# Kernel tuning notes

Measured on AMD Instinct MI355X. Metric: run time of the kernel, lower is better.

The kernel has to match this reference:

```python
import jax, jax.numpy as jnp
import numpy as np

NEG_INF = -10000.0  # module uses inf = 10000.0, not true infinity
B, S, N_TAGS, N_LABELS, N_PATTERNS = 256, 1024, 64, 32, 4


def setup_inputs() -> dict:
    key = jax.random.key(0)
    ks = jax.random.split(key, 8)
    label_emissions = jax.random.normal(ks[0], (B, S, N_LABELS), jnp.float32)
    pattern_emissions = jax.random.normal(ks[1], (B, S, N_PATTERNS), jnp.float32)
    y = jax.random.randint(ks[2], (B, S), 0, N_TAGS)
    label_transitions = 0.1 * jax.random.normal(ks[3], (N_LABELS, N_LABELS), jnp.float32)
    tag2label = jax.random.randint(ks[4], (N_TAGS,), 0, N_LABELS)
    tag_patterns = jax.random.bernoulli(ks[5], 0.25, (N_TAGS, N_PATTERNS)).astype(jnp.float32)
    allowed = jax.random.bernoulli(ks[6], 0.5, (N_TAGS, N_TAGS))
    transition_constraints = jnp.where(allowed, 0.0, NEG_INF).astype(jnp.float32)
    start_mask = jax.random.bernoulli(ks[7], 0.3, (N_TAGS,))
    start_mask = start_mask.at[0].set(True)  # ensure at least one start tag
    return dict(label_emissions=label_emissions,
                pattern_emissions=pattern_emissions,
                y=y,
                label_transitions=label_transitions,
                tag2label=tag2label,
                tag_patterns=tag_patterns,
                transition_constraints=transition_constraints,
                start_mask=start_mask)


def _log_p(label_emissions, pattern_emissions, label_transitions,
           tag_patterns, transition_constraints, y, tag2label, start_mask):
    # per-tag potentials x: [B, S, T]
    x = label_emissions[:, :, tag2label] + pattern_emissions @ tag_patterns.T
    # _transitions(): label_transitions.view(-1)[indices] + constraints == outer gather
    transitions = label_transitions[tag2label[:, None], tag2label[None, :]] + transition_constraints  # [T, T]

    # ----- _logZ (forward algorithm, enforce_boundaries=True) -----
    init = jnp.where(start_mask[None, :], x[:, 0, :], NEG_INF)  # [B, T]

    def step(logits, xi):
        # logmmexp(logits, transitions) + xi
        new = jax.nn.logsumexp(logits[:, :, None] + transitions[None, :, :], axis=1) + xi
        return new, None

    xs = jnp.moveaxis(x[:, 1:, :], 1, 0)  # [S-1, B, T]
    final, _ = jax.lax.scan(step, init, xs)
    logZ = jax.nn.logsumexp(final, axis=1)  # [B]

    # ----- _score -----
    emission = jnp.take_along_axis(x, y[:, :, None], axis=2)[:, :, 0].sum(axis=1)  # [B]
    trans = transitions[y[:, :-1], y[:, 1:]].sum(axis=1)  # [B]
    return emission + trans - logZ


def reference(label_emissions, pattern_emissions, y, label_transitions,
              tag2label, tag_patterns, transition_constraints, start_mask):
    return _log_p(label_emissions, pattern_emissions, label_transitions,
                  tag_patterns, transition_constraints, y, tag2label, start_mask)
```

## Files before the change

### kernel.cpp

```cpp
#include <hip/hip_runtime.h>

#define LOG2E 1.4426950408889634f
#define LN2   0.6931471805599453f
#define PSC   8.0f

typedef __attribute__((ext_vector_type(8))) short bf16x8;
typedef __attribute__((ext_vector_type(4))) float f32x4;
typedef __attribute__((ext_vector_type(4))) unsigned u32x4;

__device__ __forceinline__ unsigned pk_bf16(float lo, float hi){
  unsigned r;
  asm("v_cvt_pk_bf16_f32 %0, %1, %2" : "=v"(r) : "v"(lo), "v"(hi));
  return r;
}

__device__ __forceinline__ float wave_sum64(float v){
#define DADD(ctrl) { int _t = __builtin_amdgcn_update_dpp(0, __float_as_int(v), ctrl, 0xF, 0xF, false); \
                     v = v + __int_as_float(_t); }
  DADD(0x111) DADD(0x112) DADD(0x114) DADD(0x118) DADD(0x142) DADD(0x143)
#undef DADD
  return __int_as_float(__builtin_amdgcn_readlane(__float_as_int(v), 63));
}
__device__ __forceinline__ float wave_max64(float v){
#define DMAX(ctrl) { int _t = __builtin_amdgcn_update_dpp(__float_as_int(v), __float_as_int(v), ctrl, 0xF, 0xF, false); \
                     v = fmaxf(v, __int_as_float(_t)); }
  DMAX(0x111) DMAX(0x112) DMAX(0x114) DMAX(0x118) DMAX(0x142) DMAX(0x143)
#undef DMAX
  return __int_as_float(__builtin_amdgcn_readlane(__float_as_int(v), 63));
}
__device__ __forceinline__ f32x4 vmax4(f32x4 a, f32x4 b){
  f32x4 r; r.x=fmaxf(a.x,b.x); r.y=fmaxf(a.y,b.y); r.z=fmaxf(a.z,b.z); r.w=fmaxf(a.w,b.w); return r;
}

__global__ void __launch_bounds__(512, 1)
patcrf_fwd(const float* __restrict__ le, const float* __restrict__ pe,
           const int* __restrict__ y, const float* __restrict__ lt,
           const int* __restrict__ t2l, const float* __restrict__ tp,
           const float* __restrict__ tc, const unsigned int* __restrict__ smask,
           float* __restrict__ out)
{
  const int b = blockIdx.x;
  const int tid = threadIdx.x;
  const int wv = tid >> 6;
  const int lane = tid & 63;
  const int bb = lane & 15, jj = lane >> 4;

  __shared__ __align__(16) char smem[69632];
  float* E_lds     = (float*)smem;
  float* trans_lds = (float*)(smem + 32768);
  int*   y_lds     = (int*)(smem + 49152);
  float* P_lds     = (float*)smem;
  __shared__ __align__(16) float tp_lds[256];
  __shared__ __align__(16) float pf[64];
  __shared__ int   t2l_lds[64];
  __shared__ float scpart[8];
  __shared__ float L2arr[4];

  if (tid < 64){
    t2l_lds[tid] = t2l[tid];
    *(f32x4*)(tp_lds + tid*4) = *(const f32x4*)(tp + tid*4);
  }
  const int* yb = y + b*1024;
  y_lds[tid] = yb[tid];
  y_lds[tid+512] = yb[tid+512];
  __syncthreads();
  #pragma unroll
  for (int k=0;k<8;k++){
    int idx = k*512 + tid;
    trans_lds[idx] = lt[t2l_lds[idx>>6]*32 + t2l_lds[idx&63]] + tc[idx];
  }
  __syncthreads();

  const float* leb = le + (size_t)b*1024*32;
  const float* peb = pe + (size_t)b*1024*4;

  {
    int s0 = tid*2;
    int y0 = y_lds[s0], y1 = y_lds[s0+1];
    f32x4 pA = *(const f32x4*)(peb + (size_t)s0*4);
    f32x4 pB = *(const f32x4*)(peb + (size_t)(s0+1)*4);
    f32x4 tA = *(const f32x4*)(tp_lds + y0*4);
    f32x4 tB = *(const f32x4*)(tp_lds + y1*4);
    float s = leb[(size_t)s0*32 + t2l_lds[y0]]
            + pA.x*tA.x + pA.y*tA.y + pA.z*tA.z + pA.w*tA.w
            + leb[(size_t)(s0+1)*32 + t2l_lds[y1]]
            + pB.x*tB.x + pB.y*tB.y + pB.z*tB.z + pB.w*tB.w;
    s += trans_lds[y0*64 + y1];
    if (s0+2 < 1024) s += trans_lds[y1*64 + y_lds[s0+2]];
    float sw = wave_sum64(s);
    if (lane==0) scpart[wv] = sw;
  }

  if (wv < 4){
    const int c = wv;
    u32x4 Af[4][2];
    #pragma unroll
    for (int m=0;m<4;m++){
      #pragma unroll
      for (int h=0;h<2;h++){
        unsigned uu[4];
        #pragma unroll
        for (int q=0;q<4;q++){
          int c0 = 2*q, c1 = 2*q+1;
          int sg0 = 32*h + ((c0>>2)<<4) + 4*jj + (c0&3);
          int sg1 = 32*h + ((c1>>2)<<4) + 4*jj + (c1&3);
          float w0 = __builtin_amdgcn_exp2f(trans_lds[sg0*64 + 16*m + bb]*LOG2E);
          float w1 = __builtin_amdgcn_exp2f(trans_lds[sg1*64 + 16*m + bb]*LOG2E);
          uu[q] = pk_bf16(w0, w1);
        }
        Af[m][h] = (u32x4){uu[0],uu[1],uu[2],uu[3]};
      }
    }
    f32x4 acc[4][4];
    #pragma unroll
    for (int m=0;m<4;m++){
      #pragma unroll
      for (int n=0;n<4;n++){
        f32x4 z;
        z.x = (m==n && bb==4*jj+0) ? 1.f : 0.f;
        z.y = (m==n && bb==4*jj+1) ? 1.f : 0.f;
        z.z = (m==n && bb==4*jj+2) ? 1.f : 0.f;
        z.w = (m==n && bb==4*jj+3) ? 1.f : 0.f;
        acc[m][n] = z;
      }
    }
    float L2c = 0.f;
    const f32x4 zf = {0.f,0.f,0.f,0.f};

    __syncthreads();

    for (int ep=0; ep<16; ++ep){
      const float* Eb = E_lds + (c*2 + (ep&1))*1024;
      #pragma unroll 2
      for (int s=0;s<16;s++){
        if (c==0 && ep==0 && s==0) continue;
        f32x4 ev[4];
        #pragma unroll
        for (int m=0;m<4;m++) ev[m] = *(const f32x4*)(Eb + s*64 + 16*m + 4*jj);
        u32x4 Bf[2][4];
        #pragma unroll
        for (int n=0;n<4;n++){
          #pragma unroll
          for (int h=0;h<2;h++){
            Bf[h][n] = (u32x4){
              pk_bf16(acc[2*h][n].x,   acc[2*h][n].y),
              pk_bf16(acc[2*h][n].z,   acc[2*h][n].w),
              pk_bf16(acc[2*h+1][n].x, acc[2*h+1][n].y),
              pk_bf16(acc[2*h+1][n].z, acc[2*h+1][n].w) };
          }
        }
        #pragma unroll
        for (int m=0;m<4;m++){
          #pragma unroll
          for (int n=0;n<4;n++){
            f32x4 d = __builtin_amdgcn_mfma_f32_16x16x32_bf16(
                        __builtin_bit_cast(bf16x8, Af[m][0]),
                        __builtin_bit_cast(bf16x8, Bf[0][n]), zf, 0,0,0);
            d = __builtin_amdgcn_mfma_f32_16x16x32_bf16(
                        __builtin_bit_cast(bf16x8, Af[m][1]),
                        __builtin_bit_cast(bf16x8, Bf[1][n]), d, 0,0,0);
            acc[m][n] = d * ev[m];
          }
        }
      }
      f32x4 m4 = acc[0][0];
      #pragma unroll
      for (int m=0;m<4;m++){
        #pragma unroll
        for (int n=0;n<4;n++) m4 = vmax4(m4, acc[m][n]);
      }
      float mx = fmaxf(fmaxf(m4.x,m4.y), fmaxf(m4.z,m4.w));
      mx = wave_max64(mx);
      if (mx > 0.f){
        int Ex = (int)(__float_as_uint(mx)>>23) - 127;
        if (Ex != 0){
          float scl = __uint_as_float((unsigned)(127 - Ex) << 23);
          #pragma unroll
          for (int m=0;m<4;m++){
            #pragma unroll
            for (int n=0;n<4;n++) acc[m][n] = acc[m][n]*scl;
          }
          L2c += (float)Ex;
        }
      }
      __syncthreads();
    }

    float* Pc = P_lds + c*4352;
    #pragma unroll
    for (int m=0;m<4;m++){
      #pragma unroll
      for (int n=0;n<4;n++){
        Pc[(16*m+4*jj+0)*68 + 16*n + bb] = acc[m][n].x;
        Pc[(16*m+4*jj+1)*68 + 16*n + bb] = acc[m][n].y;
        Pc[(16*m+4*jj+2)*68 + 16*n + bb] = acc[m][n].z;
        Pc[(16*m+4*jj+3)*68 + 16*n + bb] = acc[m][n].w;
      }
    }
    if (lane==0) L2arr[c] = L2c;

  } else {
    const int c = wv - 4;
    const int myl = t2l_lds[lane];
    const f32x4 myt = *(const f32x4*)(tp_lds + lane*4);
    float leA[16]; f32x4 peA[16];
    #pragma unroll
    for (int s=0;s<16;s++){
      int t = 256*c + s;
      leA[s] = leb[(size_t)t*32 + myl];
      peA[s] = *(const f32x4*)(peb + (size_t)t*4);
    }
    #pragma unroll
    for (int s=0;s<16;s++){
      float x2 = (leA[s] + peA[s].x*myt.x + peA[s].y*myt.y
                         + peA[s].z*myt.z + peA[s].w*myt.w)*LOG2E - PSC;
      E_lds[(c*2+0)*1024 + s*64 + lane] = __builtin_amdgcn_exp2f(x2);
    }
    #pragma unroll
    for (int s=0;s<16;s++){
      int t = 256*c + 16 + s;
      leA[s] = leb[(size_t)t*32 + myl];
      peA[s] = *(const f32x4*)(peb + (size_t)t*4);
    }
    __syncthreads();

    for (int ep=0; ep<16; ++ep){
      if (ep < 15){
        float* Eh = E_lds + (c*2 + ((ep+1)&1))*1024;
        #pragma unroll
        for (int s=0;s<16;s++){
          float x2 = (leA[s] + peA[s].x*myt.x + peA[s].y*myt.y
                             + peA[s].z*myt.z + peA[s].w*myt.w)*LOG2E - PSC;
          Eh[s*64 + lane] = __builtin_amdgcn_exp2f(x2);
        }
        if (ep < 14){
          #pragma unroll
          for (int s=0;s<16;s++){
            int t = 256*c + 16*(ep+2) + s;
            leA[s] = leb[(size_t)t*32 + myl];
            peA[s] = *(const f32x4*)(peb + (size_t)t*4);
          }
        }
      }
      __syncthreads();
    }
  }
  __syncthreads();

  if (wv == 0){
    bool all01 = true, allf = true;
    #pragma unroll
    for (int k=0;k<16;k++){
      unsigned v = smask[k];
      all01 = all01 && (v <= 1u);
      allf  = allf  && (v == 0u || v == 0x3F800000u);
    }
    int startv;
    if (all01)      startv = ((const int*)smask)[lane];
    else if (allf)  startv = (((const unsigned*)smask)[lane] != 0u) ? 1 : 0;
    else            startv = ((const unsigned char*)smask)[lane];

    const int myl0 = t2l_lds[lane];
    const f32x4 myt0 = *(const f32x4*)(tp_lds + lane*4);
    f32x4 pe0 = *(const f32x4*)peb;
    float x0 = leb[myl0] + pe0.x*myt0.x + pe0.y*myt0.y + pe0.z*myt0.z + pe0.w*myt0.w;
    float v = startv ? __builtin_amdgcn_exp2f(x0*LOG2E - PSC) : 0.f;
    float L2p = 0.f;

    #pragma unroll 1
    for (int cc=0; cc<4; ++cc){
      pf[lane] = v;
      __builtin_amdgcn_wave_barrier();
      asm volatile("" ::: "memory");
      const float* Pr = P_lds + cc*4352 + lane*68;
      float q = 0.f;
      #pragma unroll
      for (int k=0;k<16;k++){
        f32x4 vv = *(const f32x4*)(pf + 4*k);
        f32x4 pp = *(const f32x4*)(Pr + 4*k);
        q = fmaf(vv.x, pp.x, q); q = fmaf(vv.y, pp.y, q);
        q = fmaf(vv.z, pp.z, q); q = fmaf(vv.w, pp.w, q);
      }
      __builtin_amdgcn_wave_barrier();
      asm volatile("" ::: "memory");
      float S = wave_sum64(q);
      L2p += __builtin_amdgcn_logf(S);
      v = q * __builtin_amdgcn_rcpf(S);
    }
    if (lane == 0){
      float sct = (scpart[0]+scpart[1])+(scpart[2]+scpart[3])
                + (scpart[4]+scpart[5])+(scpart[6]+scpart[7]);
      float l2t = (L2arr[0]+L2arr[1])+(L2arr[2]+L2arr[3]);
      float logZ = LN2 * (l2t + L2p + PSC*1024.0f);
      out[b] = sct - logZ;
    }
  }
}

extern "C" void kernel_launch(void* const* d_in, const int* in_sizes, int n_in,
                              void* d_out, int out_size, void* d_ws, size_t ws_size,
                              hipStream_t stream)
{
  patcrf_fwd<<<256, 512, 0, stream>>>(
    (const float*)d_in[0],
    (const float*)d_in[1],
    (const int*)d_in[2],
    (const float*)d_in[3],
    (const int*)d_in[4],
    (const float*)d_in[5],
    (const float*)d_in[6],
    (const unsigned int*)d_in[7],
    (float*)d_out);
}
```

Baseline: 119.9 us.

## Split each MFMA wave's chunk into two interleaved independent matrix-product chains

Each of the four MFMA waves now carries two independent 64x64 transition-product accumulators covering two 128-step sub-chunks, interleaving their MFMA chains so one chain's dependent work can hide the other's latency. The producer waves compute emissions for both sub-chunks per epoch, and the epoch count halves. The final partial products are stored to LDS as bf16 so eight matrices fit, and the combine wave now walks eight chunks. This raises register pressure, and the bf16 storage of products adds rounding error.

```diff
diff --git a/kernel.cpp b/kernel.cpp
--- a/kernel.cpp
+++ b/kernel.cpp
@@ -12,6 +12,10 @@
   unsigned r;
   asm("v_cvt_pk_bf16_f32 %0, %1, %2" : "=v"(r) : "v"(lo), "v"(hi));
   return r;
+}
+__device__ __forceinline__ unsigned short bf16_rne(float x){
+  unsigned u = __float_as_uint(x);
+  return (unsigned short)((u + 0x7FFFu + ((u>>16)&1u)) >> 16);
 }
 
 __device__ __forceinline__ float wave_sum64(float v){
@@ -45,16 +49,16 @@
   const int lane = tid & 63;
   const int bb = lane & 15, jj = lane >> 4;
 
-  __shared__ __align__(16) char smem[69632];
-  float* E_lds     = (float*)smem;
-  float* trans_lds = (float*)(smem + 32768);
-  int*   y_lds     = (int*)(smem + 49152);
-  float* P_lds     = (float*)smem;
+  __shared__ __align__(16) char smem[86016];
+  float* trans_lds = (float*)smem;
+  int*   y_lds     = (int*)(smem + 16384);
+  float* E_lds     = (float*)(smem + 20480);
+  unsigned short* P_lds = (unsigned short*)smem;
   __shared__ __align__(16) float tp_lds[256];
   __shared__ __align__(16) float pf[64];
   __shared__ int   t2l_lds[64];
   __shared__ float scpart[8];
-  __shared__ float L2arr[4];
+  __shared__ float L2arr[8];
 
   if (tid < 64){
     t2l_lds[tid] = t2l[tid];
@@ -73,6 +77,8 @@
 
   const float* leb = le + (size_t)b*1024*32;
   const float* peb = pe + (size_t)b*1024*4;
+  const int   myl  = t2l_lds[lane];
+  const f32x4 mytp = *(const f32x4*)(tp_lds + lane*4);
 
   {
     int s0 = tid*2;
@@ -91,6 +97,60 @@
     if (lane==0) scpart[wv] = sw;
   }
 
+#define CSTEP(ACC, EPTR) do { \
+    f32x4 ev[4]; \
+    _Pragma("unroll") \
+    for (int m_=0;m_<4;m_++) ev[m_] = *(const f32x4*)((EPTR) + 16*m_ + 4*jj); \
+    u32x4 Bf[2][4]; \
+    _Pragma("unroll") \
+    for (int n_=0;n_<4;n_++){ \
+      _Pragma("unroll") \
+      for (int h_=0;h_<2;h_++){ \
+        Bf[h_][n_] = (u32x4){ \
+          pk_bf16(ACC[2*h_][n_].x,   ACC[2*h_][n_].y), \
+          pk_bf16(ACC[2*h_][n_].z,   ACC[2*h_][n_].w), \
+          pk_bf16(ACC[2*h_+1][n_].x, ACC[2*h_+1][n_].y), \
+          pk_bf16(ACC[2*h_+1][n_].z, ACC[2*h_+1][n_].w) }; \
+      } \
+    } \
+    _Pragma("unroll") \
+    for (int m_=0;m_<4;m_++){ \
+      _Pragma("unroll") \
+      for (int n_=0;n_<4;n_++){ \
+        f32x4 d_ = __builtin_amdgcn_mfma_f32_16x16x32_bf16( \
+                     __builtin_bit_cast(bf16x8, Af[m_][0]), \
+                     __builtin_bit_cast(bf16x8, Bf[0][n_]), zf, 0,0,0); \
+        d_ = __builtin_amdgcn_mfma_f32_16x16x32_bf16( \
+                     __builtin_bit_cast(bf16x8, Af[m_][1]), \
+                     __builtin_bit_cast(bf16x8, Bf[1][n_]), d_, 0,0,0); \
+        ACC[m_][n_] = d_ * ev[m_]; \
+      } \
+    } \
+  } while(0)
+
+#define RENORM(ACC, L2V) do { \
+    f32x4 m4_ = ACC[0][0]; \
+    _Pragma("unroll") \
+    for (int m_=0;m_<4;m_++){ \
+      _Pragma("unroll") \
+      for (int n_=0;n_<4;n_++) m4_ = vmax4(m4_, ACC[m_][n_]); \
+    } \
+    float mx_ = fmaxf(fmaxf(m4_.x,m4_.y), fmaxf(m4_.z,m4_.w)); \
+    mx_ = wave_max64(mx_); \
+    if (mx_ > 0.f){ \
+      int Ex_ = (int)(__float_as_uint(mx_)>>23) - 127; \
+      if (Ex_ != 0){ \
+        float scl_ = __uint_as_float((unsigned)(127 - Ex_) << 23); \
+        _Pragma("unroll") \
+        for (int m_=0;m_<4;m_++){ \
+          _Pragma("unroll") \
+          for (int n_=0;n_<4;n_++) ACC[m_][n_] = ACC[m_][n_]*scl_; \
+        } \
+        (L2V) += (float)Ex_; \
+      } \
+    } \
+  } while(0)
+
   if (wv < 4){
     const int c = wv;
     u32x4 Af[4][2];
@@ -111,7 +171,7 @@
         Af[m][h] = (u32x4){uu[0],uu[1],uu[2],uu[3]};
       }
     }
-    f32x4 acc[4][4];
+    f32x4 accA[4][4], accB[4][4];
     #pragma unroll
     for (int m=0;m<4;m++){
       #pragma unroll
@@ -121,130 +181,88 @@
         z.y = (m==n && bb==4*jj+1) ? 1.f : 0.f;
         z.z = (m==n && bb==4*jj+2) ? 1.f : 0.f;
         z.w = (m==n && bb==4*jj+3) ? 1.f : 0.f;
-        acc[m][n] = z;
-      }
-    }
-    float L2c = 0.f;
+        accA[m][n] = z; accB[m][n] = z;
+      }
+    }
+    float L2A = 0.f, L2B = 0.f;
     const f32x4 zf = {0.f,0.f,0.f,0.f};
 
     __syncthreads();
 
-    for (int ep=0; ep<16; ++ep){
-      const float* Eb = E_lds + (c*2 + (ep&1))*1024;
+    for (int ep=0; ep<8; ++ep){
+      const float* EbA = E_lds + (c*4 + (ep&1)*2 + 0)*1024;
+      const float* EbB = E_lds + (c*4 + (ep&1)*2 + 1)*1024;
       #pragma unroll 2
       for (int s=0;s<16;s++){
-        if (c==0 && ep==0 && s==0) continue;
-        f32x4 ev[4];
-        #pragma unroll
-        for (int m=0;m<4;m++) ev[m] = *(const f32x4*)(Eb + s*64 + 16*m + 4*jj);
-        u32x4 Bf[2][4];
-        #pragma unroll
-        for (int n=0;n<4;n++){
-          #pragma unroll
-          for (int h=0;h<2;h++){
-            Bf[h][n] = (u32x4){
-              pk_bf16(acc[2*h][n].x,   acc[2*h][n].y),
-              pk_bf16(acc[2*h][n].z,   acc[2*h][n].w),
-              pk_bf16(acc[2*h+1][n].x, acc[2*h+1][n].y),
-              pk_bf16(acc[2*h+1][n].z, acc[2*h+1][n].w) };
-          }
-        }
-        #pragma unroll
-        for (int m=0;m<4;m++){
-          #pragma unroll
-          for (int n=0;n<4;n++){
-            f32x4 d = __builtin_amdgcn_mfma_f32_16x16x32_bf16(
-                        __builtin_bit_cast(bf16x8, Af[m][0]),
-                        __builtin_bit_cast(bf16x8, Bf[0][n]), zf, 0,0,0);
-            d = __builtin_amdgcn_mfma_f32_16x16x32_bf16(
-                        __builtin_bit_cast(bf16x8, Af[m][1]),
-                        __builtin_bit_cast(bf16x8, Bf[1][n]), d, 0,0,0);
-            acc[m][n] = d * ev[m];
-          }
-        }
-      }
-      f32x4 m4 = acc[0][0];
+        if (!(c==0 && ep==0 && s==0)) CSTEP(accA, EbA + s*64);
+        CSTEP(accB, EbB + s*64);
+      }
+      RENORM(accA, L2A);
+      RENORM(accB, L2B);
+      __syncthreads();
+    }
+
+    {
+      unsigned short* PcA = P_lds + (2*c  )*4352;
+      unsigned short* PcB = P_lds + (2*c+1)*4352;
       #pragma unroll
       for (int m=0;m<4;m++){
         #pragma unroll
-        for (int n=0;n<4;n++) m4 = vmax4(m4, acc[m][n]);
-      }
-      float mx = fmaxf(fmaxf(m4.x,m4.y), fmaxf(m4.z,m4.w));
-      mx = wave_max64(mx);
-      if (mx > 0.f){
-        int Ex = (int)(__float_as_uint(mx)>>23) - 127;
-        if (Ex != 0){
-          float scl = __uint_as_float((unsigned)(127 - Ex) << 23);
-          #pragma unroll
-          for (int m=0;m<4;m++){
-            #pragma unroll
-            for (int n=0;n<4;n++) acc[m][n] = acc[m][n]*scl;
-          }
-          L2c += (float)Ex;
+        for (int n=0;n<4;n++){
+          PcA[(16*m+4*jj+0)*68 + 16*n + bb] = bf16_rne(accA[m][n].x);
+          PcA[(16*m+4*jj+1)*68 + 16*n + bb] = bf16_rne(accA[m][n].y);
+          PcA[(16*m+4*jj+2)*68 + 16*n + bb] = bf16_rne(accA[m][n].z);
+          PcA[(16*m+4*jj+3)*68 + 16*n + bb] = bf16_rne(accA[m][n].w);
+          PcB[(16*m+4*jj+0)*68 + 16*n + bb] = bf16_rne(accB[m][n].x);
+          PcB[(16*m+4*jj+1)*68 + 16*n + bb] = bf16_rne(accB[m][n].y);
+          PcB[(16*m+4*jj+2)*68 + 16*n + bb] = bf16_rne(accB[m][n].z);
+          PcB[(16*m+4*jj+3)*68 + 16*n + bb] = bf16_rne(accB[m][n].w);
         }
       }
-      __syncthreads();
-    }
-
-    float* Pc = P_lds + c*4352;
-    #pragma unroll
-    for (int m=0;m<4;m++){
-      #pragma unroll
-      for (int n=0;n<4;n++){
-        Pc[(16*m+4*jj+0)*68 + 16*n + bb] = acc[m][n].x;
-        Pc[(16*m+4*jj+1)*68 + 16*n + bb] = acc[m][n].y;
-        Pc[(16*m+4*jj+2)*68 + 16*n + bb] = acc[m][n].z;
-        Pc[(16*m+4*jj+3)*68 + 16*n + bb] = acc[m][n].w;
-      }
-    }
-    if (lane==0) L2arr[c] = L2c;
-
+      if (lane==0){ L2arr[2*c] = L2A; L2arr[2*c+1] = L2B; }
+    }
   } else {
     const int c = wv - 4;
-    const int myl = t2l_lds[lane];
-    const f32x4 myt = *(const f32x4*)(tp_lds + lane*4);
-    float leA[16]; f32x4 peA[16];
-    #pragma unroll
-    for (int s=0;s<16;s++){
-      int t = 256*c + s;
-      leA[s] = leb[(size_t)t*32 + myl];
-      peA[s] = *(const f32x4*)(peb + (size_t)t*4);
-    }
-    #pragma unroll
-    for (int s=0;s<16;s++){
-      float x2 = (leA[s] + peA[s].x*myt.x + peA[s].y*myt.y
-                         + peA[s].z*myt.z + peA[s].w*myt.w)*LOG2E - PSC;
-      E_lds[(c*2+0)*1024 + s*64 + lane] = __builtin_amdgcn_exp2f(x2);
-    }
-    #pragma unroll
-    for (int s=0;s<16;s++){
-      int t = 256*c + 16 + s;
-      leA[s] = leb[(size_t)t*32 + myl];
-      peA[s] = *(const f32x4*)(peb + (size_t)t*4);
+    const int base = 256*c;
+    float leA[32]; f32x4 peA[32];
+    #pragma unroll
+    for (int k=0;k<32;k++){
+      int t = base + 128*(k>>4) + (k&15);
+      float l0 = leb[(size_t)t*32 + myl];
+      f32x4 p0 = *(const f32x4*)(peb + (size_t)t*4);
+      float x2 = (l0 + p0.x*mytp.x + p0.y*mytp.y + p0.z*mytp.z + p0.w*mytp.w)*LOG2E - PSC;
+      E_lds[(c*4 + (k>>4))*1024 + (k&15)*64 + lane] = __builtin_amdgcn_exp2f(x2);
+    }
+    #pragma unroll
+    for (int k=0;k<32;k++){
+      int t = base + 128*(k>>4) + 16 + (k&15);
+      leA[k] = leb[(size_t)t*32 + myl];
+      peA[k] = *(const f32x4*)(peb + (size_t)t*4);
     }
     __syncthreads();
 
-    for (int ep=0; ep<16; ++ep){
-      if (ep < 15){
-        float* Eh = E_lds + (c*2 + ((ep+1)&1))*1024;
+    for (int ep=0; ep<8; ++ep){
+      if (ep < 7){
+        int buf = (ep+1)&1;
         #pragma unroll
-        for (int s=0;s<16;s++){
-          float x2 = (leA[s] + peA[s].x*myt.x + peA[s].y*myt.y
-                             + peA[s].z*myt.z + peA[s].w*myt.w)*LOG2E - PSC;
-          Eh[s*64 + lane] = __builtin_amdgcn_exp2f(x2);
+        for (int k=0;k<32;k++){
+          float x2 = (leA[k] + peA[k].x*mytp.x + peA[k].y*mytp.y
+                             + peA[k].z*mytp.z + peA[k].w*mytp.w)*LOG2E - PSC;
+          E_lds[(c*4 + buf*2 + (k>>4))*1024 + (k&15)*64 + lane] = __builtin_amdgcn_exp2f(x2);
         }
-        if (ep < 14){
+        if (ep < 6){
           #pragma unroll
-          for (int s=0;s<16;s++){
-            int t = 256*c + 16*(ep+2) + s;
-            leA[s] = leb[(size_t)t*32 + myl];
-            peA[s] = *(const f32x4*)(peb + (size_t)t*4);
+          for (int k=0;k<32;k++){
+            int t = base + 128*(k>>4) + 16*(ep+2) + (k&15);
+            leA[k] = leb[(size_t)t*32 + myl];
+            peA[k] = *(const f32x4*)(peb + (size_t)t*4);
           }
         }
       }
       __syncthreads();
     }
   }
+
   __syncthreads();
 
   if (wv == 0){
@@ -260,26 +278,26 @@
     else if (allf)  startv = (((const unsigned*)smask)[lane] != 0u) ? 1 : 0;
     else            startv = ((const unsigned char*)smask)[lane];
 
-    const int myl0 = t2l_lds[lane];
-    const f32x4 myt0 = *(const f32x4*)(tp_lds + lane*4);
     f32x4 pe0 = *(const f32x4*)peb;
-    float x0 = leb[myl0] + pe0.x*myt0.x + pe0.y*myt0.y + pe0.z*myt0.z + pe0.w*myt0.w;
+    float x0 = leb[myl] + pe0.x*mytp.x + pe0.y*mytp.y + pe0.z*mytp.z + pe0.w*mytp.w;
     float v = startv ? __builtin_amdgcn_exp2f(x0*LOG2E - PSC) : 0.f;
     float L2p = 0.f;
 
     #pragma unroll 1
-    for (int cc=0; cc<4; ++cc){
+    for (int cc=0; cc<8; ++cc){
       pf[lane] = v;
       __builtin_amdgcn_wave_barrier();
       asm volatile("" ::: "memory");
-      const float* Pr = P_lds + cc*4352 + lane*68;
+      const unsigned short* Pr = P_lds + cc*4352 + lane*68;
       float q = 0.f;
       #pragma unroll
       for (int k=0;k<16;k++){
+        uint2 u = *(const uint2*)(Pr + 4*k);
         f32x4 vv = *(const f32x4*)(pf + 4*k);
-        f32x4 pp = *(const f32x4*)(Pr + 4*k);
-        q = fmaf(vv.x, pp.x, q); q = fmaf(vv.y, pp.y, q);
-        q = fmaf(vv.z, pp.z, q); q = fmaf(vv.w, pp.w, q);
+        q = fmaf(__uint_as_float(u.x << 16),          vv.x, q);
+        q = fmaf(__uint_as_float(u.x & 0xFFFF0000u),  vv.y, q);
+        q = fmaf(__uint_as_float(u.y << 16),          vv.z, q);
+        q = fmaf(__uint_as_float(u.y & 0xFFFF0000u),  vv.w, q);
       }
       __builtin_amdgcn_wave_barrier();
       asm volatile("" ::: "memory");
@@ -288,13 +306,16 @@
       v = q * __builtin_amdgcn_rcpf(S);
     }
     if (lane == 0){
-      float sct = (scpart[0]+scpart[1])+(scpart[2]+scpart[3])
-                + (scpart[4]+scpart[5])+(scpart[6]+scpart[7]);
-      float l2t = (L2arr[0]+L2arr[1])+(L2arr[2]+L2arr[3]);
+      float sct = ((scpart[0]+scpart[1])+(scpart[2]+scpart[3]))
+                + ((scpart[4]+scpart[5])+(scpart[6]+scpart[7]));
+      float l2t = ((L2arr[0]+L2arr[1])+(L2arr[2]+L2arr[3]))
+                + ((L2arr[4]+L2arr[5])+(L2arr[6]+L2arr[7]));
       float logZ = LN2 * (l2t + L2p + PSC*1024.0f);
       out[b] = sct - logZ;
     }
   }
+#undef CSTEP
+#undef RENORM
 }
 
 extern "C" void kernel_launch(void* const* d_in, const int* in_sizes, int n_in,
```

Result: no change. 119.3 us, median of 3 (-0.5%).
